# Optimization experiments

Measured on AMD Instinct MI355X. Metric: run time of the kernel, lower is better.

## Reference

```python
import jax, jax.numpy as jnp
import numpy as np

N_IMG = 512            # size_image (square)
N_NEO = 510            # size_neo = size_image - 2
NUM_CLASSES = 32
NUM_HIDDEN = 64
C_STATE = NUM_HIDDEN + NUM_CLASSES   # input_dim - img_channels = 96
OUT_DIM = C_STATE + 2                # num_hidden + num_classes + act_channels
ITERS = 50
THRESH = 0.0007
N_ACTIVE = N_IMG - 2


def setup_inputs() -> dict:
    key = jax.random.key(0)
    ks = jax.random.split(key, 5)
    img = jax.random.uniform(ks[0], (N_IMG, N_IMG, 1), dtype=jnp.float32)
    # Conv2D(1, 3x3, stride 1) over state  -> kernel HWIO [3,3,C_STATE,1]
    comms_w = jax.random.normal(ks[1], (3, 3, C_STATE, 1), jnp.float32) * 0.05
    comms_b = jnp.zeros((1,), jnp.float32)
    # Conv2D(1, 3x3, stride 3) over gathered image -> [3,3,1,1]
    perc_w = jax.random.normal(ks[2], (3, 3, 1, 1), jnp.float32) * 0.05
    perc_b = jnp.zeros((1,), jnp.float32)
    # Conv2D(OUT_DIM, 1x1, sigmoid) -> [1,1,2,OUT_DIM]
    out_w = jax.random.normal(ks[3], (1, 1, 2, OUT_DIM), jnp.float32) * 0.05
    out_b = jnp.zeros((OUT_DIM,), jnp.float32)
    return {"img": img, "comms_w": comms_w, "comms_b": comms_b,
            "perc_w": perc_w, "perc_b": perc_b, "out_w": out_w, "out_b": out_b}


def _nca_forward(img, comms_w, comms_b, perc_w, perc_b, out_w, out_b):
    # initial perception matrix: evenly spread positions over active area
    base = jnp.rint(jnp.arange(N_NEO) * (N_ACTIVE - 1) / max(N_NEO - 1, 1)).astype(jnp.int32)
    perc0 = jnp.stack(jnp.meshgrid(base, base, indexing="ij"), axis=-1)  # [N_neo, M_neo, 2]
    state0 = jnp.zeros((N_NEO + 2, N_NEO + 2, C_STATE), img.dtype)
    offs = jnp.arange(3, dtype=jnp.int32)
    w11 = out_w[0, 0]  # [2, OUT_DIM]

    def step(carry, _):
        state, perc = carry
        # expand + gather_mine fused: 3x3 neighborhood at each perception position
        xi = perc[:, None, :, None, 0] + offs[None, :, None, None]   # [N,3,M,1]
        yj = perc[:, None, :, None, 1] + offs[None, None, None, :]   # [N,1,M,3]
        gathered = img[xi, yj, :]                                    # [N,3,M,3,1]
        # 3x3 stride-3 conv == weighted sum over the gathered 3x3 patch
        percep = jnp.einsum("nimjc,ijck->nmk", gathered, perc_w) + perc_b  # [N,M,1]
        # 3x3 stride-1 valid conv over the padded state
        comms = jax.lax.conv_general_dilated(
            state[None], comms_w, (1, 1), "VALID",
            dimension_numbers=("NHWC", "HWIO", "NHWC"))[0] + comms_b       # [N,M,1]
        full = jnp.concatenate([comms, percep], axis=-1)                   # [N,M,2]
        outputs = jax.nn.sigmoid(jnp.einsum("nmc,ck->nmk", full, w11) + out_b)
        state = state.at[1:1 + N_NEO, 1:1 + N_NEO, :].add(outputs[:, :, :C_STATE])
        # movement: threshold-round action to {-1,0,1}, then clip positions
        action = outputs[:, :, -2:]
        delta = jnp.where(action < -THRESH, -1,
                          jnp.where(action > THRESH, 1, 0)).astype(jnp.int32)
        perc = jnp.clip(perc + delta, 0, N_ACTIVE - 1)
        return (state, perc), None

    (state, _), _ = jax.lax.scan(step, (state0, perc0), None, length=ITERS)
    return state[1:1 + N_NEO, 1:1 + N_NEO, -NUM_CLASSES:]


def reference(img, comms_w, comms_b, perc_w, perc_b, out_w, out_b):
    return _nca_forward(img, comms_w, comms_b, perc_w, perc_b, out_w, out_b)
```

## Files before the change

### kernel.cpp

```cpp
#include <hip/hip_runtime.h>


#define NIMG   512
#define NNEO   510
#define NCELL  (NNEO * NNEO)
#define TILE   32
#define MARGIN 5
#define EXT    (TILE + 2 * MARGIN)
#define EXTC   (EXT * EXT)
#define RING   (EXTC - TILE * TILE)
#define KIT    5
#define NCHUNK 10
#define SP     (NNEO + 2 * MARGIN + 2)
#define CLIPHI 509
#define NTHREADS 1024
#define NCA_THRESH 0.0007f
#define NEG_L2E (-1.44269504088896341f)

#define CMIN   (-32.0f)
#define INV_DC 8.0f
#define NCI    512
#define PMIN   (-2.0f)
#define INV_DP 8.0f
#define NPI    32
#define NPP    36
#define TQ     12
#define TBL_F32 ((NCI + 1) * NPP * TQ)

using v2f = __attribute__((ext_vector_type(2))) float;

__device__ __forceinline__ v2f pk_fma(v2f a, v2f b, v2f c) {
    return __builtin_elementwise_fma(a, b, c);
}

struct Cell {
    float C;
    int   x, y;
    int   ln, lm;
    int   act;
};

__global__ void nca_build(const float* __restrict__ cw,
                          const float* __restrict__ ow,
                          const float* __restrict__ ob,
                          float* __restrict__ sw,
                          float* __restrict__ table) {
    const int t = (int)(blockIdx.x * 256 + threadIdx.x);
    if (blockIdx.x == 0 && threadIdx.x < 98) {
        const int i = (int)threadIdx.x;
        sw[i]       = ow[i]      * NEG_L2E;
        sw[128 + i] = ow[98 + i] * NEG_L2E;
        sw[256 + i] = ob[i]      * NEG_L2E;
    }
    const int npts = (NCI + 1) * (NPI + 1);
    if (t >= npts * TQ) return;
    const int q  = t % TQ;
    const int pt = t / TQ;
    const int ci = pt / (NPI + 1);
    const int pi = pt % (NPI + 1);
    float F = 0.0f;
    if (q < 9) {
        const float c = CMIN + (float)ci * (1.0f / INV_DC);
        const float p = PMIN + (float)pi * (1.0f / INV_DP);
        for (int k = 0; k < 96; ++k) {
            const float arg = fmaf(c, ow[k], fmaf(p, ow[98 + k], ob[k])) * NEG_L2E;
            const float s = __builtin_amdgcn_rcpf(1.0f + __builtin_amdgcn_exp2f(arg));
            F = fmaf(s, cw[q * 96 + k], F);
        }
    }
    table[(ci * NPP + pi) * TQ + q] = F;
}

template<bool OWNED>
__device__ __forceinline__ void g_phase(
    Cell& S, int j,
    const float* __restrict__ img,
    const float* __restrict__ pw,
    float pbias, float cbias,
    const float* __restrict__ sw,
    const float* __restrict__ table,
    float* Gs,
    v2f* acc2)
{
    if (!OWNED) {
        if (S.ln < j || S.ln >= EXT - j || S.lm < j || S.lm >= EXT - j) return;
    }
    if (!S.act) return;

    const float* ip = img + S.x * NIMG + S.y;
    float p = pbias;
    #pragma unroll
    for (int i = 0; i < 3; ++i)
        #pragma unroll
        for (int jj = 0; jj < 3; ++jj)
            p = fmaf(ip[i * NIMG + jj], pw[i * 3 + jj], p);

    const float c = S.C + cbias;

    const float cf  = fminf(fmaxf((c - CMIN) * INV_DC, 0.0f), (float)NCI - 0.001f);
    const float pf  = fminf(fmaxf((p - PMIN) * INV_DP, 0.0f), (float)NPI - 0.001f);
    const float cif = floorf(cf), pif = floorf(pf);
    const float fc  = cf - cif,  fp  = pf - pif;
    const int   b4  = (((int)cif * NPP + (int)pif) * TQ) >> 2;
    const int   b4c = b4 + ((NPP * TQ) >> 2);
    const float4* T = (const float4*)table;

    const float4 A0 = T[b4],     A1 = T[b4 + 1],  A2q = T[b4 + 2];
    const float4 B0 = T[b4 + 3], B1 = T[b4 + 4],  B2q = T[b4 + 5];
    const float4 C0 = T[b4c],    C1 = T[b4c + 1], C2q = T[b4c + 2];
    const float4 D0 = T[b4c + 3], D1 = T[b4c + 4], D2q = T[b4c + 5];

    auto bi = [&](float a, float b, float cq, float d) {
        const float e = fmaf(fp, b - a, a);
        const float f = fmaf(fp, d - cq, cq);
        return fmaf(fc, f - e, e);
    };

    const int ci_cell = S.ln * EXT + S.lm;
    Gs[0 * EXTC + ci_cell] = bi(A0.x, B0.x, C0.x, D0.x);
    Gs[1 * EXTC + ci_cell] = bi(A0.y, B0.y, C0.y, D0.y);
    Gs[2 * EXTC + ci_cell] = bi(A0.z, B0.z, C0.z, D0.z);
    Gs[3 * EXTC + ci_cell] = bi(A0.w, B0.w, C0.w, D0.w);
    Gs[4 * EXTC + ci_cell] = bi(A1.x, B1.x, C1.x, D1.x);
    Gs[5 * EXTC + ci_cell] = bi(A1.y, B1.y, C1.y, D1.y);
    Gs[6 * EXTC + ci_cell] = bi(A1.z, B1.z, C1.z, D1.z);
    Gs[7 * EXTC + ci_cell] = bi(A1.w, B1.w, C1.w, D1.w);
    Gs[8 * EXTC + ci_cell] = bi(A2q.x, B2q.x, C2q.x, D2q.x);

    const v2f cc = {c, c};
    const v2f pp = {p, p};
    const v2f* A2 = (const v2f*)(sw);
    const v2f* B2 = (const v2f*)(sw + 128);
    const v2f* D2 = (const v2f*)(sw + 256);

    if (OWNED) {
        #pragma unroll
        for (int kb = 32; kb < 48; ++kb) {
            const v2f arg = pk_fma(cc, A2[kb], pk_fma(pp, B2[kb], D2[kb]));
            v2f e2;
            e2.x = __builtin_amdgcn_exp2f(arg.x);
            e2.y = __builtin_amdgcn_exp2f(arg.y);
            const v2f o2 = e2 + 1.0f;
            v2f s;
            s.x = __builtin_amdgcn_rcpf(o2.x);
            s.y = __builtin_amdgcn_rcpf(o2.y);
            acc2[kb - 32] += s;
        }
    }

    const v2f argA = pk_fma(cc, A2[48], pk_fma(pp, B2[48], D2[48]));
    const float s96 = __builtin_amdgcn_rcpf(1.0f + __builtin_amdgcn_exp2f(argA.x));
    const float s97 = __builtin_amdgcn_rcpf(1.0f + __builtin_amdgcn_exp2f(argA.y));
    const int dx = (s96 < -NCA_THRESH) ? -1 : ((s96 > NCA_THRESH) ? 1 : 0);
    const int dy = (s97 < -NCA_THRESH) ? -1 : ((s97 > NCA_THRESH) ? 1 : 0);
    S.x = min(max(S.x + dx, 0), CLIPHI);
    S.y = min(max(S.y + dy, 0), CLIPHI);
}

template<bool OWNED>
__device__ __forceinline__ void c_phase(Cell& S, int j, const float* Gs) {
    if (!OWNED) {
        if (S.ln < j + 1 || S.ln >= EXT - j - 1 ||
            S.lm < j + 1 || S.lm >= EXT - j - 1) return;
    }
    if (!S.act) return;
    const int base = (S.ln - 1) * EXT + (S.lm - 1);
    float sum = 0.f;
    #pragma unroll
    for (int i = 0; i < 3; ++i)
        #pragma unroll
        for (int jj = 0; jj < 3; ++jj)
            sum += Gs[(i * 3 + jj) * EXTC + base + i * EXT + jj];
    S.C += sum;
}

__global__ __launch_bounds__(NTHREADS, 4) void nca_chunk(
    const float* __restrict__ img, const float* __restrict__ cb,
    const float* __restrict__ pw,  const float* __restrict__ pb,
    const float* __restrict__ sw,  const float* __restrict__ table,
    float* __restrict__ Cst,
    int*   __restrict__ XYst,
    float* __restrict__ out,
    int chunk)
{
    __shared__ float Gs[9 * EXTC];

    const int tid = (int)threadIdx.x;
    const int bn = (int)blockIdx.y, bm = (int)blockIdx.x;

    for (int i = tid; i < 9 * EXTC; i += NTHREADS) Gs[i] = 0.f;

    Cell S0, S1;
    S0.ln = MARGIN + (tid >> 5);
    S0.lm = MARGIN + (tid & 31);
    const bool has1 = (tid < RING);
    {
        const int TOP = MARGIN * EXT;
        int r = tid;
        if (r < TOP)          { S1.ln = r / EXT;                        S1.lm = r % EXT; }
        else if (r < 2 * TOP) { S1.ln = EXT - MARGIN + (r - TOP) / EXT; S1.lm = (r - TOP) % EXT; }
        else {
            const int rr = r - 2 * TOP;
            S1.ln = MARGIN + rr / (2 * MARGIN);
            const int cc2 = rr % (2 * MARGIN);
            S1.lm = (cc2 < MARGIN) ? cc2 : cc2 + TILE;
        }
    }

    auto initCell = [&](Cell& S) {
        const int gn = bn * TILE - MARGIN + S.ln;
        const int gm = bm * TILE - MARGIN + S.lm;
        S.act = (gn >= 0 && gn < NNEO && gm >= 0 && gm < NNEO) ? 1 : 0;
        if (chunk == 0) {
            S.C = 0.f; S.x = S.act ? gn : 0; S.y = S.act ? gm : 0;
        } else if (S.act) {
            const int si = (bn * TILE + S.ln) * SP + bm * TILE + S.lm;
            S.C = Cst[si];
            const int xy = XYst[si];
            S.x = xy >> 16; S.y = xy & 0xffff;
        } else {
            S.C = 0.f; S.x = 0; S.y = 0;
        }
    };
    initCell(S0);
    if (has1) initCell(S1);
    else { S1.act = 0; S1.C = 0.f; S1.x = 0; S1.y = 0; S1.ln = 0; S1.lm = 0; }

    const int gn0 = bn * TILE + (tid >> 5);
    const int gm0 = bm * TILE + (tid & 31);
    v2f acc2[16];
    if (chunk > 0 && S0.act) {
        const float4* i4 = (const float4*)(out + (size_t)(gn0 * NNEO + gm0) * 32);
        #pragma unroll
        for (int v = 0; v < 8; ++v) {
            const float4 t = i4[v];
            acc2[2 * v]     = (v2f){t.x, t.y};
            acc2[2 * v + 1] = (v2f){t.z, t.w};
        }
    } else {
        #pragma unroll
        for (int k = 0; k < 16; ++k) acc2[k] = (v2f){0.f, 0.f};
    }

    const float cbias = cb[0], pbias = pb[0];
    __syncthreads();

    #pragma unroll 1
    for (int j = 0; j < KIT; ++j) {
        g_phase<true>(S0, j, img, pw, pbias, cbias, sw, table, Gs, acc2);
        if (has1) g_phase<false>(S1, j, img, pw, pbias, cbias, sw, table, Gs, nullptr);
        __syncthreads();
        c_phase<true>(S0, j, Gs);
        if (has1) c_phase<false>(S1, j, Gs);
        __syncthreads();
    }

    if (S0.act) {
        const int si = (bn * TILE + S0.ln) * SP + bm * TILE + S0.lm;
        Cst[si]  = S0.C;
        XYst[si] = (S0.x << 16) | S0.y;
        float4* o4 = (float4*)(out + (size_t)(gn0 * NNEO + gm0) * 32);
        #pragma unroll
        for (int v = 0; v < 8; ++v)
            o4[v] = make_float4(acc2[2 * v].x, acc2[2 * v].y,
                                acc2[2 * v + 1].x, acc2[2 * v + 1].y);
    }
}

extern "C" void kernel_launch(void* const* d_in, const int* in_sizes, int n_in,
                              void* d_out, int out_size, void* d_ws, size_t ws_size,
                              hipStream_t stream) {
    const float* img = (const float*)d_in[0];
    const float* cw  = (const float*)d_in[1];
    const float* cb  = (const float*)d_in[2];
    const float* pw  = (const float*)d_in[3];
    const float* pb  = (const float*)d_in[4];
    const float* ow  = (const float*)d_in[5];
    const float* ob  = (const float*)d_in[6];
    float* out = (float*)d_out;

    char* ws = (char*)d_ws;
    float* Cst   = (float*)(ws);
    int*   XYst  = (int*)(ws + (size_t)SP * SP * 4);
    float* sw    = (float*)(ws + (size_t)SP * SP * 8);
    float* table = (float*)(ws + (size_t)SP * SP * 8 + 1536);

    {
        const int total = (NCI + 1) * (NPI + 1) * TQ;
        nca_build<<<dim3((total + 255) / 256, 1, 1), dim3(256, 1, 1), 0, stream>>>(
            cw, ow, ob, sw, table);
    }

    const dim3 grid(16, 16, 1);
    const dim3 block(NTHREADS, 1, 1);
    for (int chunk = 0; chunk < NCHUNK; ++chunk) {
        nca_chunk<<<grid, block, 0, stream>>>(
            img, cb, pw, pb, sw, table, Cst, XYst, out, chunk);
    }
}
```

Measured before the change: 445.7 us.

## Defer class-channel sigmoid accumulation to a final pass over stored (c,p) history

Each owned cell in the chunk kernel now records its (c,p) pair per iteration into a history buffer instead of computing 32 class sigmoids inline. A new final kernel replays all 50 steps per cell to accumulate the class outputs. The 2D interpolation table is re-laid out so each q entry holds its four bilinear corners in one float4, cutting corner loads per cell from twelve to nine. This shortens the synchronized iteration loop, but it adds a large history buffer that must be written and then read back, plus one more launch.

```diff
diff --git a/kernel.cpp b/kernel.cpp
--- a/kernel.cpp
+++ b/kernel.cpp
@@ -25,12 +25,14 @@
 #define NPI    32
 #define NPP    36
 #define TQ     12
-#define TBL_F32 ((NCI + 1) * NPP * TQ)
 
 using v2f = __attribute__((ext_vector_type(2))) float;
 
 __device__ __forceinline__ v2f pk_fma(v2f a, v2f b, v2f c) {
     return __builtin_elementwise_fma(a, b, c);
+}
+__device__ __forceinline__ float sigf(float x) {
+    return __builtin_amdgcn_rcpf(1.0f + __builtin_amdgcn_exp2f(x * NEG_L2E));
 }
 
 struct Cell {
@@ -44,7 +46,7 @@
                           const float* __restrict__ ow,
                           const float* __restrict__ ob,
                           float* __restrict__ sw,
-                          float* __restrict__ table) {
+                          float4* __restrict__ table4) {
     const int t = (int)(blockIdx.x * 256 + threadIdx.x);
     if (blockIdx.x == 0 && threadIdx.x < 98) {
         const int i = (int)threadIdx.x;
@@ -52,23 +54,35 @@
         sw[128 + i] = ow[98 + i] * NEG_L2E;
         sw[256 + i] = ob[i]      * NEG_L2E;
     }
-    const int npts = (NCI + 1) * (NPI + 1);
-    if (t >= npts * TQ) return;
-    const int q  = t % TQ;
-    const int pt = t / TQ;
-    const int ci = pt / (NPI + 1);
-    const int pi = pt % (NPI + 1);
-    float F = 0.0f;
-    if (q < 9) {
-        const float c = CMIN + (float)ci * (1.0f / INV_DC);
-        const float p = PMIN + (float)pi * (1.0f / INV_DP);
-        for (int k = 0; k < 96; ++k) {
-            const float arg = fmaf(c, ow[k], fmaf(p, ow[98 + k], ob[k])) * NEG_L2E;
-            const float s = __builtin_amdgcn_rcpf(1.0f + __builtin_amdgcn_exp2f(arg));
-            F = fmaf(s, cw[q * 96 + k], F);
+    if (t >= NCI * NPI) return;
+    const int ci = t >> 5;
+    const int pi = t & 31;
+    const float c0 = CMIN + (float)ci * 0.125f, c1 = c0 + 0.125f;
+    const float p0 = PMIN + (float)pi * 0.125f, p1 = p0 + 0.125f;
+
+    float F00[9], F01[9], F10[9], F11[9];
+    #pragma unroll
+    for (int q = 0; q < 9; ++q) { F00[q]=0.f; F01[q]=0.f; F10[q]=0.f; F11[q]=0.f; }
+
+    for (int k = 0; k < 96; ++k) {
+        const float a = ow[k], b = ow[98 + k], d = ob[k];
+        const float s00 = sigf(fmaf(c0, a, fmaf(p0, b, d)));
+        const float s01 = sigf(fmaf(c0, a, fmaf(p1, b, d)));
+        const float s10 = sigf(fmaf(c1, a, fmaf(p0, b, d)));
+        const float s11 = sigf(fmaf(c1, a, fmaf(p1, b, d)));
+        #pragma unroll
+        for (int q = 0; q < 9; ++q) {
+            const float w = cw[q * 96 + k];
+            F00[q] = fmaf(s00, w, F00[q]);
+            F01[q] = fmaf(s01, w, F01[q]);
+            F10[q] = fmaf(s10, w, F10[q]);
+            F11[q] = fmaf(s11, w, F11[q]);
         }
     }
-    table[(ci * NPP + pi) * TQ + q] = F;
+    const int base = (ci * NPP + pi) * TQ;
+    #pragma unroll
+    for (int q = 0; q < 9; ++q)
+        table4[base + q] = make_float4(F00[q], F01[q], F10[q], F11[q]);
 }
 
 template<bool OWNED>
@@ -78,9 +92,10 @@
     const float* __restrict__ pw,
     float pbias, float cbias,
     const float* __restrict__ sw,
-    const float* __restrict__ table,
+    const float4* __restrict__ table4,
     float* Gs,
-    v2f* acc2)
+    float2* __restrict__ histRow,
+    int cellIdx)
 {
     if (!OWNED) {
         if (S.ln < j || S.ln >= EXT - j || S.lm < j || S.lm >= EXT - j) return;
@@ -97,57 +112,28 @@
 
     const float c = S.C + cbias;
 
+    if (OWNED) histRow[cellIdx] = make_float2(c, p);
+
     const float cf  = fminf(fmaxf((c - CMIN) * INV_DC, 0.0f), (float)NCI - 0.001f);
     const float pf  = fminf(fmaxf((p - PMIN) * INV_DP, 0.0f), (float)NPI - 0.001f);
     const float cif = floorf(cf), pif = floorf(pf);
     const float fc  = cf - cif,  fp  = pf - pif;
-    const int   b4  = (((int)cif * NPP + (int)pif) * TQ) >> 2;
-    const int   b4c = b4 + ((NPP * TQ) >> 2);
-    const float4* T = (const float4*)table;
-
-    const float4 A0 = T[b4],     A1 = T[b4 + 1],  A2q = T[b4 + 2];
-    const float4 B0 = T[b4 + 3], B1 = T[b4 + 4],  B2q = T[b4 + 5];
-    const float4 C0 = T[b4c],    C1 = T[b4c + 1], C2q = T[b4c + 2];
-    const float4 D0 = T[b4c + 3], D1 = T[b4c + 4], D2q = T[b4c + 5];
-
-    auto bi = [&](float a, float b, float cq, float d) {
-        const float e = fmaf(fp, b - a, a);
-        const float f = fmaf(fp, d - cq, cq);
-        return fmaf(fc, f - e, e);
-    };
+    const float4* T = table4 + (((int)cif * NPP + (int)pif) * TQ);
 
     const int ci_cell = S.ln * EXT + S.lm;
-    Gs[0 * EXTC + ci_cell] = bi(A0.x, B0.x, C0.x, D0.x);
-    Gs[1 * EXTC + ci_cell] = bi(A0.y, B0.y, C0.y, D0.y);
-    Gs[2 * EXTC + ci_cell] = bi(A0.z, B0.z, C0.z, D0.z);
-    Gs[3 * EXTC + ci_cell] = bi(A0.w, B0.w, C0.w, D0.w);
-    Gs[4 * EXTC + ci_cell] = bi(A1.x, B1.x, C1.x, D1.x);
-    Gs[5 * EXTC + ci_cell] = bi(A1.y, B1.y, C1.y, D1.y);
-    Gs[6 * EXTC + ci_cell] = bi(A1.z, B1.z, C1.z, D1.z);
-    Gs[7 * EXTC + ci_cell] = bi(A1.w, B1.w, C1.w, D1.w);
-    Gs[8 * EXTC + ci_cell] = bi(A2q.x, B2q.x, C2q.x, D2q.x);
+    #pragma unroll
+    for (int q = 0; q < 9; ++q) {
+        const float4 v = T[q];
+        const float lo = fmaf(fp, v.y - v.x, v.x);
+        const float hi = fmaf(fp, v.w - v.z, v.z);
+        Gs[q * EXTC + ci_cell] = fmaf(fc, hi - lo, lo);
+    }
 
     const v2f cc = {c, c};
     const v2f pp = {p, p};
     const v2f* A2 = (const v2f*)(sw);
     const v2f* B2 = (const v2f*)(sw + 128);
     const v2f* D2 = (const v2f*)(sw + 256);
-
-    if (OWNED) {
-        #pragma unroll
-        for (int kb = 32; kb < 48; ++kb) {
-            const v2f arg = pk_fma(cc, A2[kb], pk_fma(pp, B2[kb], D2[kb]));
-            v2f e2;
-            e2.x = __builtin_amdgcn_exp2f(arg.x);
-            e2.y = __builtin_amdgcn_exp2f(arg.y);
-            const v2f o2 = e2 + 1.0f;
-            v2f s;
-            s.x = __builtin_amdgcn_rcpf(o2.x);
-            s.y = __builtin_amdgcn_rcpf(o2.y);
-            acc2[kb - 32] += s;
-        }
-    }
-
     const v2f argA = pk_fma(cc, A2[48], pk_fma(pp, B2[48], D2[48]));
     const float s96 = __builtin_amdgcn_rcpf(1.0f + __builtin_amdgcn_exp2f(argA.x));
     const float s97 = __builtin_amdgcn_rcpf(1.0f + __builtin_amdgcn_exp2f(argA.y));
@@ -177,10 +163,10 @@
 __global__ __launch_bounds__(NTHREADS, 4) void nca_chunk(
     const float* __restrict__ img, const float* __restrict__ cb,
     const float* __restrict__ pw,  const float* __restrict__ pb,
-    const float* __restrict__ sw,  const float* __restrict__ table,
+    const float* __restrict__ sw,  const float4* __restrict__ table4,
     float* __restrict__ Cst,
     int*   __restrict__ XYst,
-    float* __restrict__ out,
+    float2* __restrict__ hist,
     int chunk)
 {
     __shared__ float Gs[9 * EXTC];
@@ -228,27 +214,16 @@
 
     const int gn0 = bn * TILE + (tid >> 5);
     const int gm0 = bm * TILE + (tid & 31);
-    v2f acc2[16];
-    if (chunk > 0 && S0.act) {
-        const float4* i4 = (const float4*)(out + (size_t)(gn0 * NNEO + gm0) * 32);
-        #pragma unroll
-        for (int v = 0; v < 8; ++v) {
-            const float4 t = i4[v];
-            acc2[2 * v]     = (v2f){t.x, t.y};
-            acc2[2 * v + 1] = (v2f){t.z, t.w};
-        }
-    } else {
-        #pragma unroll
-        for (int k = 0; k < 16; ++k) acc2[k] = (v2f){0.f, 0.f};
-    }
+    const int cellIdx = gn0 * NNEO + gm0;
 
     const float cbias = cb[0], pbias = pb[0];
     __syncthreads();
 
     #pragma unroll 1
     for (int j = 0; j < KIT; ++j) {
-        g_phase<true>(S0, j, img, pw, pbias, cbias, sw, table, Gs, acc2);
-        if (has1) g_phase<false>(S1, j, img, pw, pbias, cbias, sw, table, Gs, nullptr);
+        float2* histRow = hist + (size_t)(chunk * KIT + j) * NCELL;
+        g_phase<true >(S0, j, img, pw, pbias, cbias, sw, table4, Gs, histRow, cellIdx);
+        if (has1) g_phase<false>(S1, j, img, pw, pbias, cbias, sw, table4, Gs, nullptr, 0);
         __syncthreads();
         c_phase<true>(S0, j, Gs);
         if (has1) c_phase<false>(S1, j, Gs);
@@ -259,12 +234,47 @@
         const int si = (bn * TILE + S0.ln) * SP + bm * TILE + S0.lm;
         Cst[si]  = S0.C;
         XYst[si] = (S0.x << 16) | S0.y;
-        float4* o4 = (float4*)(out + (size_t)(gn0 * NNEO + gm0) * 32);
+    }
+}
+
+__global__ __launch_bounds__(256) void nca_final(
+    const float2* __restrict__ hist,
+    const float* __restrict__ sw,
+    float* __restrict__ out)
+{
+    const int cell = (int)(blockIdx.x * 256 + threadIdx.x);
+    if (cell >= NCELL) return;
+    const v2f* A2 = (const v2f*)(sw);
+    const v2f* B2 = (const v2f*)(sw + 128);
+    const v2f* D2 = (const v2f*)(sw + 256);
+
+    v2f acc2[16];
+    #pragma unroll
+    for (int k = 0; k < 16; ++k) acc2[k] = (v2f){0.f, 0.f};
+
+    #pragma unroll 2
+    for (int t = 0; t < NCHUNK * KIT; ++t) {
+        const float2 cp = hist[(size_t)t * NCELL + cell];
+        const v2f cc = {cp.x, cp.x};
+        const v2f pp = {cp.y, cp.y};
         #pragma unroll
-        for (int v = 0; v < 8; ++v)
-            o4[v] = make_float4(acc2[2 * v].x, acc2[2 * v].y,
-                                acc2[2 * v + 1].x, acc2[2 * v + 1].y);
-    }
+        for (int kb = 0; kb < 16; ++kb) {
+            const v2f arg = pk_fma(cc, A2[32 + kb], pk_fma(pp, B2[32 + kb], D2[32 + kb]));
+            v2f e;
+            e.x = __builtin_amdgcn_exp2f(arg.x);
+            e.y = __builtin_amdgcn_exp2f(arg.y);
+            const v2f o = e + 1.0f;
+            v2f s;
+            s.x = __builtin_amdgcn_rcpf(o.x);
+            s.y = __builtin_amdgcn_rcpf(o.y);
+            acc2[kb] += s;
+        }
+    }
+    float4* o4 = (float4*)(out + (size_t)cell * 32);
+    #pragma unroll
+    for (int v = 0; v < 8; ++v)
+        o4[v] = make_float4(acc2[2 * v].x, acc2[2 * v].y,
+                            acc2[2 * v + 1].x, acc2[2 * v + 1].y);
 }
 
 extern "C" void kernel_launch(void* const* d_in, const int* in_sizes, int n_in,
@@ -280,21 +290,21 @@
     float* out = (float*)d_out;
 
     char* ws = (char*)d_ws;
-    float* Cst   = (float*)(ws);
-    int*   XYst  = (int*)(ws + (size_t)SP * SP * 4);
-    float* sw    = (float*)(ws + (size_t)SP * SP * 8);
-    float* table = (float*)(ws + (size_t)SP * SP * 8 + 1536);
-
-    {
-        const int total = (NCI + 1) * (NPI + 1) * TQ;
-        nca_build<<<dim3((total + 255) / 256, 1, 1), dim3(256, 1, 1), 0, stream>>>(
-            cw, ow, ob, sw, table);
-    }
+    float*  Cst    = (float*)(ws);
+    int*    XYst   = (int*)(ws + 1089936);
+    float*  sw     = (float*)(ws + 2179872);
+    float4* table4 = (float4*)(ws + 2181408);
+    float2* hist   = (float2*)(ws + 5720352);
+
+    nca_build<<<dim3((NCI * NPI + 255) / 256, 1, 1), dim3(256, 1, 1), 0, stream>>>(
+        cw, ow, ob, sw, table4);
 
     const dim3 grid(16, 16, 1);
     const dim3 block(NTHREADS, 1, 1);
     for (int chunk = 0; chunk < NCHUNK; ++chunk) {
         nca_chunk<<<grid, block, 0, stream>>>(
-            img, cb, pw, pb, sw, table, Cst, XYst, out, chunk);
-    }
-}
+            img, cb, pw, pb, sw, table4, Cst, XYst, hist, chunk);
+    }
+    nca_final<<<dim3((NCELL + 255) / 256, 1, 1), dim3(256, 1, 1), 0, stream>>>(
+        hist, sw, out);
+}
```

New measurement: 373.7 us. 16.1% less time.
